# Performance work log

Hardware: AMD Instinct MI355X
Metric: run time of the kernel (lower is better)

Reference implementation:

```python
import jax, jax.numpy as jnp
import numpy as np
from jax import lax

NUM_ITER = 10  # num_iterations
NUM_CLASSES = 21


def _avg_pool(x, k):
    # PyTorch F.avg_pool2d with stride=1, padding=k//2, count_include_pad=True:
    # zero-pad, sum over kxk window, divide by k*k.
    p = k // 2
    s = lax.reduce_window(x, 0.0, lax.add, (1, 1, k, k), (1, 1, 1, 1),
                          [(0, 0), (0, 0), (p, p), (p, p)])
    return s / float(k * k)


def _edge_weight(image):
    # grayscale -> sobel gradients -> exp(-|grad|)
    gray = 0.299 * image[:, 0:1] + 0.587 * image[:, 1:2] + 0.114 * image[:, 2:3]
    sx = jnp.array([[-1, 0, 1], [-2, 0, 2], [-1, 0, 1]], dtype=image.dtype).reshape(1, 1, 3, 3)
    sy = jnp.array([[-1, -2, -1], [0, 0, 0], [1, 2, 1]], dtype=image.dtype).reshape(1, 1, 3, 3)
    dn = ('NCHW', 'OIHW', 'NCHW')
    gx = lax.conv_general_dilated(gray, sx, (1, 1), [(1, 1), (1, 1)], dimension_numbers=dn)
    gy = lax.conv_general_dilated(gray, sy, (1, 1), [(1, 1), (1, 1)], dimension_numbers=dn)
    mag = jnp.sqrt(gx ** 2 + gy ** 2 + 1e-6)
    return jnp.exp(-mag)  # [B,1,H,W]


def setup_inputs() -> dict:
    key = jax.random.key(0)
    k1, k2 = jax.random.split(key)
    B, C, H, W = 8, NUM_CLASSES, 512, 512
    unary = jax.random.normal(k1, (B, C, H, W), dtype=jnp.float32)
    image = jax.random.uniform(k2, (B, 3, H, W), dtype=jnp.float32)
    compatibility = jnp.eye(C, dtype=jnp.float32)
    spatial_weight = jnp.asarray(3.0, dtype=jnp.float32)
    bilateral_weight = jnp.asarray(5.0, dtype=jnp.float32)
    return {"unary": unary, "image": image, "compatibility": compatibility,
            "spatial_weight": spatial_weight, "bilateral_weight": bilateral_weight}


def reference(unary, image, compatibility, spatial_weight, bilateral_weight):
    # edge weights depend only on the image -> compute once (identical math each iter)
    edge = _edge_weight(image)                  # [B,1,H,W]
    norm = _avg_pool(edge, 3) + 1e-6            # bilateral normalizer
    sw = jnp.maximum(spatial_weight, 0.0)
    bw = jnp.maximum(bilateral_weight, 0.0)

    Q = jax.nn.softmax(unary, axis=1)
    for _ in range(NUM_ITER):
        Q_spatial = _avg_pool(Q, 5)
        Q_bilateral = _avg_pool(Q * edge, 3) / norm
        messages = sw * Q_spatial + bw * Q_bilateral
        # bmm(compat [C,C], messages [B,C,HW]) == einsum over class dim
        compat = jnp.einsum('cd,bdhw->bchw', compatibility, messages)
        Q = jax.nn.softmax(unary - compat, axis=1)
    return Q
```

## Files before the change

kernel.cpp:

```cpp
#include <hip/hip_runtime.h>
#include <hip/hip_fp16.h>

#define PLANE 262144
#define NC 21
#define NB 8
#define NPIX (NB*PLANE)

__device__ __forceinline__ float2 h2f(unsigned int u) {
  union { unsigned int u; __half2 h; } x; x.u = u;
  return __half22float2(x.h);
}
__device__ __forceinline__ unsigned int f2h(float a, float b) {
  union { unsigned int u; __half2 h; } x;
  x.h = __floats2half2_rn(a, b);
  return x.u;
}

__global__ __launch_bounds__(256)
void k_edge(const float* __restrict__ img, __half* __restrict__ edge16) {
  int id = blockIdx.x*256 + threadIdx.x;
  int b = id >> 18;
  int rem = id & (PLANE-1);
  int y = rem >> 9, x = rem & 511;
  const float* ib = img + (size_t)b*3*PLANE;
  float g[3][3];
#pragma unroll
  for (int dy=0; dy<3; ++dy)
#pragma unroll
    for (int dx=0; dx<3; ++dx) {
      int yy = y+dy-1, xx = x+dx-1;
      float v = 0.f;
      if (yy>=0 && yy<512 && xx>=0 && xx<512) {
        int o = (yy<<9)|xx;
        v = 0.299f*ib[o] + 0.587f*ib[o+PLANE] + 0.114f*ib[o+2*PLANE];
      }
      g[dy][dx]=v;
    }
  float gxv = (g[0][2]-g[0][0]) + 2.f*(g[1][2]-g[1][0]) + (g[2][2]-g[2][0]);
  float gyv = (g[2][0]-g[0][0]) + 2.f*(g[2][1]-g[0][1]) + (g[2][2]-g[0][2]);
  float mag = sqrtf(gxv*gxv + gyv*gyv + 1e-6f);
  edge16[id] = __float2half(__expf(-mag));
}

__global__ __launch_bounds__(256)
void k_rnorm(const __half* __restrict__ edge16, float* __restrict__ rnorm) {
  int id = blockIdx.x*256 + threadIdx.x;
  int b = id >> 18;
  int rem = id & (PLANE-1);
  int y = rem >> 9, x = rem & 511;
  const __half* eb = edge16 + (size_t)b*PLANE;
  float s = 0.f;
#pragma unroll
  for (int dy=-1; dy<=1; ++dy)
#pragma unroll
    for (int dx=-1; dx<=1; ++dx) {
      int yy = y+dy, xx = x+dx;
      if (yy>=0 && yy<512 && xx>=0 && xx<512) s += __half2float(eb[(yy<<9)|xx]);
    }
  rnorm[id] = 1.f/(s*(1.f/9.f) + 1e-6f);
}

__global__ void k_flag(const float* __restrict__ compat, int* __restrict__ flag) {
  __shared__ int ok;
  if (threadIdx.x==0) ok = 1;
  __syncthreads();
  int bad = 0;
  for (int i = threadIdx.x; i < NC*NC; i += 256) {
    float exp = ((i/NC) == (i%NC)) ? 1.f : 0.f;
    if (compat[i] != exp) bad = 1;
  }
  if (bad) atomicAnd(&ok, 0);
  __syncthreads();
  if (threadIdx.x==0) flag[0] = ok;
}

__global__ __launch_bounds__(256)
void k_cvt(const float* __restrict__ u, __half* __restrict__ u16) {
  size_t q = (size_t)blockIdx.x*256 + threadIdx.x;
  float4 v = reinterpret_cast<const float4*>(u)[q];
  uint2 w; w.x = f2h(v.x, v.y); w.y = f2h(v.z, v.w);
  reinterpret_cast<uint2*>(u16)[q] = w;
}

__global__ __launch_bounds__(256)
void k_softmax0(const float* __restrict__ unary, __half* __restrict__ Y) {
  int q = blockIdx.x*256 + threadIdx.x;
  int b = q >> 16;
  int rem = q & 65535;
  size_t base = (size_t)b*NC*(PLANE>>2) + rem;
  const float4* up = reinterpret_cast<const float4*>(unary);
  float v[NC][4];
  float mx0=-3e38f,mx1=-3e38f,mx2=-3e38f,mx3=-3e38f;
#pragma unroll
  for (int c=0;c<NC;++c) {
    float4 t = up[base + (size_t)c*(PLANE>>2)];
    v[c][0]=t.x; v[c][1]=t.y; v[c][2]=t.z; v[c][3]=t.w;
    mx0=fmaxf(mx0,t.x); mx1=fmaxf(mx1,t.y); mx2=fmaxf(mx2,t.z); mx3=fmaxf(mx3,t.w);
  }
  float s0=0,s1=0,s2=0,s3=0;
#pragma unroll
  for (int c=0;c<NC;++c) {
    float e0=__expf(v[c][0]-mx0), e1=__expf(v[c][1]-mx1);
    float e2=__expf(v[c][2]-mx2), e3=__expf(v[c][3]-mx3);
    v[c][0]=e0; v[c][1]=e1; v[c][2]=e2; v[c][3]=e3;
    s0+=e0; s1+=e1; s2+=e2; s3+=e3;
  }
  float r0=1.f/s0, r1=1.f/s1, r2=1.f/s2, r3=1.f/s3;
  uint2* yp = reinterpret_cast<uint2*>(Y);
#pragma unroll
  for (int c=0;c<NC;++c) {
    uint2 w; w.x=f2h(v[c][0]*r0, v[c][1]*r1); w.y=f2h(v[c][2]*r2, v[c][3]*r3);
    yp[base + (size_t)c*(PLANE>>2)] = w;
  }
}


#define LOAD_U2(c, u0,u1) \
  float u0,u1; \
  if (U16) { unsigned int w_ = reinterpret_cast<const unsigned int*>(uptr)[hbase + (size_t)(c)*ch]; \
    float2 t_=h2f(w_); u0=t_.x; u1=t_.y; } \
  else { float2 v_ = reinterpret_cast<const float2*>(uptr)[hbase + (size_t)(c)*ch]; \
    u0=v_.x; u1=v_.y; }

#define CROW 72
#define TROWS 12
#define CTILE (TROWS*CROW)

template<bool U16, bool OUTF32>
__global__ __launch_bounds__(256)
void k_iter(const __half* __restrict__ Qin,
            void* __restrict__ Qout,
            const void* __restrict__ uptr,
            const __half* __restrict__ edge16,
            const float* __restrict__ rnorm,
            const float* __restrict__ swp,
            const float* __restrict__ bwp,
            const float* __restrict__ compat,
            const int* __restrict__ flag)
{
  __shared__ __half qbuf[2][CTILE];
  __shared__ __half et[CTILE];
  __shared__ float l0[NC][256];
  __shared__ float l1[NC][256];

  const int tid = threadIdx.x;
  const int tx = tid & 31;
  const int ty = tid >> 5;
  const int x0 = blockIdx.x << 6;
  const int y0 = blockIdx.y << 3;
  const int b  = blockIdx.z;

  const int slot = tid;
  const int sr = slot / 18;
  const int si = slot - sr*18;
  const int sy = y0 - 2 + sr;
  const int sx = x0 - 4 + (si<<2);
  const bool sact = (slot < 216);
  const bool sval = sact && (sy>=0) && (sy<512) && (sx>=0) && (sx<512);
  const int  goff = (sy<<9) + sx;
  const int  loff = sr*CROW + (si<<2);

  const int gy  = y0 + ty;
  const int gx  = x0 + (tx<<1);
  const int pix = (gy<<9) | gx;

  const float2 rn = *reinterpret_cast<const float2*>(rnorm + (size_t)b*PLANE + pix);
  const float sw  = fmaxf(swp[0], 0.f);
  const float bw  = fmaxf(bwp[0], 0.f);
  const int fl = flag[0];

  const size_t hbase = (((size_t)b*NC*PLANE) + (size_t)pix) >> 1;
  const size_t ch = PLANE >> 1;

  const __half* qb = Qin + (size_t)b*NC*PLANE;
  unsigned int ucur = 0; float2 ufcur = make_float2(0.f,0.f);
  if (U16) ucur = reinterpret_cast<const unsigned int*>(uptr)[hbase];
  else     ufcur = reinterpret_cast<const float2*>(uptr)[hbase];
  {
    const __half* ep = edge16 + (size_t)b*PLANE;
    uint2 we = make_uint2(0u, 0u);
    uint2 w0 = make_uint2(0u, 0u);
    if (sval) {
      we = *reinterpret_cast<const uint2*>(ep + goff);
      w0 = *reinterpret_cast<const uint2*>(qb + goff);
    }
    if (sact) {
      *reinterpret_cast<uint2*>(et + loff) = we;
      *reinterpret_cast<uint2*>(qbuf[0] + loff) = w0;
    }
  }
  __syncthreads();

  const float csw = sw * 0.04f;
  const float b9  = bw * (1.f/9.f);
  const float cb0 = b9*rn.x, cb1 = b9*rn.y;

  const int lx2 = (tx<<1) + 2;

  float ew[3][4];
#pragma unroll
  for (int dy=0;dy<3;++dy) {
    const unsigned int* erow = reinterpret_cast<const unsigned int*>(et + (ty+1+dy)*CROW + lx2);
    float2 e0 = h2f(erow[0]);
    float2 e1 = h2f(erow[1]);
    float2 e2 = h2f(erow[2]);
    ew[dy][0]=e0.y; ew[dy][1]=e1.x; ew[dy][2]=e1.y; ew[dy][3]=e2.x;
  }

  float mx0=-3e38f, mx1=-3e38f;

#pragma unroll
  for (int c=0;c<NC;++c) {
    uint2 wn = make_uint2(0u, 0u);
    unsigned int un = 0; float2 unf = make_float2(0.f,0.f);
    if (c+1 < NC) {
      if (sval) wn = *reinterpret_cast<const uint2*>(qb + (size_t)(c+1)*PLANE + goff);
      if (U16) un = reinterpret_cast<const unsigned int*>(uptr)[hbase + (size_t)(c+1)*ch];
      else     unf = reinterpret_cast<const float2*>(uptr)[hbase + (size_t)(c+1)*ch];
    }

    const __half* qrow0 = qbuf[c&1] + ty*CROW + lx2;
    float cs0=0,cs1=0,cs2=0,cs3=0,cs4=0,cs5=0;
    float ce0=0,ce1=0,ce2=0,ce3=0;
#pragma unroll
    for (int dy=0;dy<5;++dy) {
      const unsigned int* qrow = reinterpret_cast<const unsigned int*>(qrow0 + dy*CROW);
      float2 t0 = h2f(qrow[0]);
      float2 t1 = h2f(qrow[1]);
      float2 t2 = h2f(qrow[2]);
      cs0+=t0.x; cs1+=t0.y; cs2+=t1.x; cs3+=t1.y; cs4+=t2.x; cs5+=t2.y;
      if (dy>=1 && dy<=3) {
        ce0 += t0.y*ew[dy-1][0];
        ce1 += t1.x*ew[dy-1][1];
        ce2 += t1.y*ew[dy-1][2];
        ce3 += t2.x*ew[dy-1][3];
      }
    }
    float v0 = cs0+cs1+cs2+cs3+cs4;
    float v1 = v0 - cs0 + cs5;
    float w0 = ce0+ce1+ce2;
    float w1 = ce1+ce2+ce3;
    float m0 = csw*v0 + cb0*w0;
    float m1 = csw*v1 + cb1*w1;

    float u0c, u1c;
    if (U16) { float2 t = h2f(ucur); u0c=t.x; u1c=t.y; }
    else     { u0c=ufcur.x; u1c=ufcur.y; }
    float lv0, lv1;
    if (fl) {
      lv0 = u0c - m0; lv1 = u1c - m1;
      mx0 = fmaxf(mx0, lv0); mx1 = fmaxf(mx1, lv1);
    } else {
      lv0 = m0; lv1 = m1;
    }
    l0[c][tid] = lv0;
    l1[c][tid] = lv1;

    if (c+1 < NC) {
      if (sact) *reinterpret_cast<uint2*>(qbuf[(c+1)&1] + loff) = wn;
      __syncthreads();
    }
    ucur = un; ufcur = unf;
  }

  if (fl) {
    float s0=0.f, s1=0.f;
#pragma unroll
    for (int c=0;c<NC;++c) {
      float e0=__expf(l0[c][tid]-mx0), e1=__expf(l1[c][tid]-mx1);
      l0[c][tid]=e0; l1[c][tid]=e1;
      s0+=e0; s1+=e1;
    }
    float r0=1.f/s0, r1=1.f/s1;
#pragma unroll
    for (int c=0;c<NC;++c) {
      float o0=l0[c][tid]*r0, o1=l1[c][tid]*r1;
      if (OUTF32) {
        reinterpret_cast<float2*>(Qout)[hbase + (size_t)c*ch] = make_float2(o0,o1);
      } else {
        reinterpret_cast<unsigned int*>(Qout)[hbase + (size_t)c*ch] = f2h(o0,o1);
      }
    }
  } else {
    float mxa=-3e38f, mxb=-3e38f;
#pragma unroll 1
    for (int c=0;c<NC;++c) {
      float a0=0.f,a1=0.f;
#pragma unroll
      for (int d=0;d<NC;++d) { float cf=compat[c*NC+d]; a0+=cf*l0[d][tid]; a1+=cf*l1[d][tid]; }
      LOAD_U2(c, u0,u1)
      mxa=fmaxf(mxa,u0-a0); mxb=fmaxf(mxb,u1-a1);
    }
    float s0=0.f,s1=0.f;
#pragma unroll 1
    for (int c=0;c<NC;++c) {
      float a0=0.f,a1=0.f;
#pragma unroll
      for (int d=0;d<NC;++d) { float cf=compat[c*NC+d]; a0+=cf*l0[d][tid]; a1+=cf*l1[d][tid]; }
      LOAD_U2(c, u0,u1)
      s0+=__expf(u0-a0-mxa); s1+=__expf(u1-a1-mxb);
    }
    float r0=1.f/s0, r1=1.f/s1;
#pragma unroll 1
    for (int c=0;c<NC;++c) {
      float a0=0.f,a1=0.f;
#pragma unroll
      for (int d=0;d<NC;++d) { float cf=compat[c*NC+d]; a0+=cf*l0[d][tid]; a1+=cf*l1[d][tid]; }
      LOAD_U2(c, u0,u1)
      float o0=__expf(u0-a0-mxa)*r0, o1=__expf(u1-a1-mxb)*r1;
      if (OUTF32) {
        reinterpret_cast<float2*>(Qout)[hbase + (size_t)c*ch] = make_float2(o0,o1);
      } else {
        reinterpret_cast<unsigned int*>(Qout)[hbase + (size_t)c*ch] = f2h(o0,o1);
      }
    }
  }
}

extern "C" void kernel_launch(void* const* d_in, const int* in_sizes, int n_in,
                              void* d_out, int out_size, void* d_ws, size_t ws_size,
                              hipStream_t stream)
{
  const float* unary  = (const float*)d_in[0];
  const float* image  = (const float*)d_in[1];
  const float* compat = (const float*)d_in[2];
  const float* swp    = (const float*)d_in[3];
  const float* bwp    = (const float*)d_in[4];

  char* ws = (char*)d_ws;
  __half* X      = (__half*)(ws + 0);
  __half* edge16 = (__half*)(ws + 88080384);
  float*  rnorm  = (float*) (ws + 92274688);
  int*    flag   = (int*)   (ws + 100663296);
  __half* u16    = (__half*)(ws + 100663552);
  if (ws_size < (size_t)100663552) return;
  const bool use_u16 = (ws_size >= (size_t)188743936);

  __half* Y  = (__half*)d_out;
  float* out = (float*)d_out;

  k_edge   <<<dim3(8192), dim3(256), 0, stream>>>(image, edge16);
  k_rnorm  <<<dim3(8192), dim3(256), 0, stream>>>(edge16, rnorm);
  k_flag   <<<dim3(1),    dim3(256), 0, stream>>>(compat, flag);
  if (use_u16) k_cvt<<<dim3(43008), dim3(256), 0, stream>>>(unary, u16);
  k_softmax0<<<dim3(2048), dim3(256), 0, stream>>>(unary, Y);

  const void* up = use_u16 ? (const void*)u16 : (const void*)unary;
  dim3 gi(8, 64, NB), bi(256);
  for (int it = 1; it <= 10; ++it) {
    const __half* qin = (it & 1) ? Y : X;
    if (it == 10) {
      if (use_u16) k_iter<true , true ><<<gi,bi,0,stream>>>(qin,(void*)out,up,edge16,rnorm,swp,bwp,compat,flag);
      else         k_iter<false, true ><<<gi,bi,0,stream>>>(qin,(void*)out,up,edge16,rnorm,swp,bwp,compat,flag);
    } else {
      void* qout = (it & 1) ? (void*)X : (void*)Y;
      if (use_u16) k_iter<true , false><<<gi,bi,0,stream>>>(qin,qout,up,edge16,rnorm,swp,bwp,compat,flag);
      else         k_iter<false, false><<<gi,bi,0,stream>>>(qin,qout,up,edge16,rnorm,swp,bwp,compat,flag);
    }
  }
}
```

Before: 1.311 ms.

## Process class channels in pairs with double-buffered tiles and packed half2 sums

```diff
diff --git a/kernel.cpp b/kernel.cpp
--- a/kernel.cpp
+++ b/kernel.cpp
@@ -125,6 +125,41 @@
 #define CROW 72
 #define TROWS 12
 #define CTILE (TROWS*CROW)
+
+#define COMPUTE_CH(c, buf, uu, uf) do { \
+    const __half* qrow0_ = (buf) + ty*CROW + lx2; \
+    __half2 a0_ = __float2half2_rn(0.f); \
+    __half2 a1_ = a0_, a2_ = a0_; \
+    float ce0=0.f,ce1=0.f,ce2=0.f,ce3=0.f; \
+    _Pragma("unroll") \
+    for (int dy=0;dy<5;++dy) { \
+      const __half2* qrow = reinterpret_cast<const __half2*>(qrow0_ + dy*CROW); \
+      __half2 q0=qrow[0], q1=qrow[1], q2=qrow[2]; \
+      a0_ = __hadd2(a0_, q0); a1_ = __hadd2(a1_, q1); a2_ = __hadd2(a2_, q2); \
+      if (dy>=1 && dy<=3) { \
+        ce0 += __high2float(q0)*ew[dy-1][0]; \
+        ce1 += __low2float (q1)*ew[dy-1][1]; \
+        ce2 += __high2float(q1)*ew[dy-1][2]; \
+        ce3 += __low2float (q2)*ew[dy-1][3]; \
+      } \
+    } \
+    float cs0=__low2float(a0_), cs1=__high2float(a0_); \
+    float cs2=__low2float(a1_), cs3=__high2float(a1_); \
+    float cs4=__low2float(a2_), cs5=__high2float(a2_); \
+    float v0 = cs0+cs1+cs2+cs3+cs4; \
+    float v1 = v0 - cs0 + cs5; \
+    float w0 = ce0+ce1+ce2; \
+    float w1 = ce1+ce2+ce3; \
+    float m0 = csw*v0 + cb0*w0; \
+    float m1 = csw*v1 + cb1*w1; \
+    float u0c,u1c; \
+    if (U16) { float2 t_=h2f(uu); u0c=t_.x; u1c=t_.y; } \
+    else     { u0c=(uf).x; u1c=(uf).y; } \
+    float lv0, lv1; \
+    if (fl) { lv0=u0c-m0; lv1=u1c-m1; mx0=fmaxf(mx0,lv0); mx1=fmaxf(mx1,lv1); } \
+    else    { lv0=m0; lv1=m1; } \
+    lsm[c][tid] = make_float2(lv0, lv1); \
+  } while(0)
 
 template<bool U16, bool OUTF32>
 __global__ __launch_bounds__(256)
@@ -138,10 +173,9 @@
             const float* __restrict__ compat,
             const int* __restrict__ flag)
 {
-  __shared__ __half qbuf[2][CTILE];
+  __shared__ __half qbuf[2][2][CTILE];
   __shared__ __half et[CTILE];
-  __shared__ float l0[NC][256];
-  __shared__ float l1[NC][256];
+  __shared__ float2 lsm[NC][256];
 
   const int tid = threadIdx.x;
   const int tx = tid & 31;
@@ -173,20 +207,26 @@
   const size_t ch = PLANE >> 1;
 
   const __half* qb = Qin + (size_t)b*NC*PLANE;
-  unsigned int ucur = 0; float2 ufcur = make_float2(0.f,0.f);
-  if (U16) ucur = reinterpret_cast<const unsigned int*>(uptr)[hbase];
-  else     ufcur = reinterpret_cast<const float2*>(uptr)[hbase];
+  unsigned int uc0=0, uc1=0; float2 uf0=make_float2(0.f,0.f), uf1=uf0;
+  if (U16) {
+    uc0 = reinterpret_cast<const unsigned int*>(uptr)[hbase];
+    uc1 = reinterpret_cast<const unsigned int*>(uptr)[hbase + ch];
+  } else {
+    uf0 = reinterpret_cast<const float2*>(uptr)[hbase];
+    uf1 = reinterpret_cast<const float2*>(uptr)[hbase + ch];
+  }
   {
     const __half* ep = edge16 + (size_t)b*PLANE;
-    uint2 we = make_uint2(0u, 0u);
-    uint2 w0 = make_uint2(0u, 0u);
+    uint2 we = make_uint2(0u,0u), w0 = we, w1 = we;
     if (sval) {
       we = *reinterpret_cast<const uint2*>(ep + goff);
       w0 = *reinterpret_cast<const uint2*>(qb + goff);
+      w1 = *reinterpret_cast<const uint2*>(qb + PLANE + goff);
     }
     if (sact) {
       *reinterpret_cast<uint2*>(et + loff) = we;
-      *reinterpret_cast<uint2*>(qbuf[0] + loff) = w0;
+      *reinterpret_cast<uint2*>(qbuf[0][0] + loff) = w0;
+      *reinterpret_cast<uint2*>(qbuf[0][1] + loff) = w1;
     }
   }
   __syncthreads();
@@ -210,71 +250,49 @@
   float mx0=-3e38f, mx1=-3e38f;
 
 #pragma unroll
-  for (int c=0;c<NC;++c) {
-    uint2 wn = make_uint2(0u, 0u);
-    unsigned int un = 0; float2 unf = make_float2(0.f,0.f);
-    if (c+1 < NC) {
-      if (sval) wn = *reinterpret_cast<const uint2*>(qb + (size_t)(c+1)*PLANE + goff);
-      if (U16) un = reinterpret_cast<const unsigned int*>(uptr)[hbase + (size_t)(c+1)*ch];
-      else     unf = reinterpret_cast<const float2*>(uptr)[hbase + (size_t)(c+1)*ch];
-    }
-
-    const __half* qrow0 = qbuf[c&1] + ty*CROW + lx2;
-    float cs0=0,cs1=0,cs2=0,cs3=0,cs4=0,cs5=0;
-    float ce0=0,ce1=0,ce2=0,ce3=0;
-#pragma unroll
-    for (int dy=0;dy<5;++dy) {
-      const unsigned int* qrow = reinterpret_cast<const unsigned int*>(qrow0 + dy*CROW);
-      float2 t0 = h2f(qrow[0]);
-      float2 t1 = h2f(qrow[1]);
-      float2 t2 = h2f(qrow[2]);
-      cs0+=t0.x; cs1+=t0.y; cs2+=t1.x; cs3+=t1.y; cs4+=t2.x; cs5+=t2.y;
-      if (dy>=1 && dy<=3) {
-        ce0 += t0.y*ew[dy-1][0];
-        ce1 += t1.x*ew[dy-1][1];
-        ce2 += t1.y*ew[dy-1][2];
-        ce3 += t2.x*ew[dy-1][3];
+  for (int cp=0; cp<11; ++cp) {
+    const int c0 = 2*cp, c1 = 2*cp+1;
+
+    uint2 wn0 = make_uint2(0u,0u), wn1 = wn0;
+    unsigned int un0=0, un1=0; float2 unf0=make_float2(0.f,0.f), unf1=unf0;
+    if (c0+2 < NC) {
+      if (sval) wn0 = *reinterpret_cast<const uint2*>(qb + (size_t)(c0+2)*PLANE + goff);
+      if (U16) un0 = reinterpret_cast<const unsigned int*>(uptr)[hbase + (size_t)(c0+2)*ch];
+      else     unf0 = reinterpret_cast<const float2*>(uptr)[hbase + (size_t)(c0+2)*ch];
+    }
+    if (c1+2 < NC) {
+      if (sval) wn1 = *reinterpret_cast<const uint2*>(qb + (size_t)(c1+2)*PLANE + goff);
+      if (U16) un1 = reinterpret_cast<const unsigned int*>(uptr)[hbase + (size_t)(c1+2)*ch];
+      else     unf1 = reinterpret_cast<const float2*>(uptr)[hbase + (size_t)(c1+2)*ch];
+    }
+
+    COMPUTE_CH(c0, qbuf[cp&1][0], uc0, uf0);
+    if (c1 < NC) COMPUTE_CH(c1, qbuf[cp&1][1], uc1, uf1);
+
+    if (c0+2 < NC) {
+      if (sact) {
+        *reinterpret_cast<uint2*>(qbuf[(cp+1)&1][0] + loff) = wn0;
+        if (c1+2 < NC) *reinterpret_cast<uint2*>(qbuf[(cp+1)&1][1] + loff) = wn1;
       }
-    }
-    float v0 = cs0+cs1+cs2+cs3+cs4;
-    float v1 = v0 - cs0 + cs5;
-    float w0 = ce0+ce1+ce2;
-    float w1 = ce1+ce2+ce3;
-    float m0 = csw*v0 + cb0*w0;
-    float m1 = csw*v1 + cb1*w1;
-
-    float u0c, u1c;
-    if (U16) { float2 t = h2f(ucur); u0c=t.x; u1c=t.y; }
-    else     { u0c=ufcur.x; u1c=ufcur.y; }
-    float lv0, lv1;
-    if (fl) {
-      lv0 = u0c - m0; lv1 = u1c - m1;
-      mx0 = fmaxf(mx0, lv0); mx1 = fmaxf(mx1, lv1);
-    } else {
-      lv0 = m0; lv1 = m1;
-    }
-    l0[c][tid] = lv0;
-    l1[c][tid] = lv1;
-
-    if (c+1 < NC) {
-      if (sact) *reinterpret_cast<uint2*>(qbuf[(c+1)&1] + loff) = wn;
       __syncthreads();
     }
-    ucur = un; ufcur = unf;
+    uc0=un0; uc1=un1; uf0=unf0; uf1=unf1;
   }
 
   if (fl) {
     float s0=0.f, s1=0.f;
 #pragma unroll
     for (int c=0;c<NC;++c) {
-      float e0=__expf(l0[c][tid]-mx0), e1=__expf(l1[c][tid]-mx1);
-      l0[c][tid]=e0; l1[c][tid]=e1;
+      float2 lv = lsm[c][tid];
+      float e0=__expf(lv.x-mx0), e1=__expf(lv.y-mx1);
+      lsm[c][tid]=make_float2(e0,e1);
       s0+=e0; s1+=e1;
     }
     float r0=1.f/s0, r1=1.f/s1;
 #pragma unroll
     for (int c=0;c<NC;++c) {
-      float o0=l0[c][tid]*r0, o1=l1[c][tid]*r1;
+      float2 ev = lsm[c][tid];
+      float o0=ev.x*r0, o1=ev.y*r1;
       if (OUTF32) {
         reinterpret_cast<float2*>(Qout)[hbase + (size_t)c*ch] = make_float2(o0,o1);
       } else {
@@ -287,7 +305,7 @@
     for (int c=0;c<NC;++c) {
       float a0=0.f,a1=0.f;
 #pragma unroll
-      for (int d=0;d<NC;++d) { float cf=compat[c*NC+d]; a0+=cf*l0[d][tid]; a1+=cf*l1[d][tid]; }
+      for (int d=0;d<NC;++d) { float cf=compat[c*NC+d]; float2 lv=lsm[d][tid]; a0+=cf*lv.x; a1+=cf*lv.y; }
       LOAD_U2(c, u0,u1)
       mxa=fmaxf(mxa,u0-a0); mxb=fmaxf(mxb,u1-a1);
     }
@@ -296,7 +314,7 @@
     for (int c=0;c<NC;++c) {
       float a0=0.f,a1=0.f;
 #pragma unroll
-      for (int d=0;d<NC;++d) { float cf=compat[c*NC+d]; a0+=cf*l0[d][tid]; a1+=cf*l1[d][tid]; }
+      for (int d=0;d<NC;++d) { float cf=compat[c*NC+d]; float2 lv=lsm[d][tid]; a0+=cf*lv.x; a1+=cf*lv.y; }
       LOAD_U2(c, u0,u1)
       s0+=__expf(u0-a0-mxa); s1+=__expf(u1-a1-mxb);
     }
@@ -305,7 +323,7 @@
     for (int c=0;c<NC;++c) {
       float a0=0.f,a1=0.f;
 #pragma unroll
-      for (int d=0;d<NC;++d) { float cf=compat[c*NC+d]; a0+=cf*l0[d][tid]; a1+=cf*l1[d][tid]; }
+      for (int d=0;d<NC;++d) { float cf=compat[c*NC+d]; float2 lv=lsm[d][tid]; a0+=cf*lv.x; a1+=cf*lv.y; }
       LOAD_U2(c, u0,u1)
       float o0=__expf(u0-a0-mxa)*r0, o1=__expf(u1-a1-mxb)*r1;
       if (OUTF32) {
```

Measured after the change: 1.173 ms. 1.12x faster.
